# Kernel optimization log

Measured on AMD Instinct MI355X. Metric: run time of the kernel, lower is better.

The kernel has to match this reference:

```python
import jax, jax.numpy as jnp
import numpy as np

DIM = 2048
D_INNER = 2048
B = 4
T = 4096
INIT_DECAY = 0.5


def setup_inputs() -> dict:
    key = jax.random.key(0)
    k1, k2, k3 = jax.random.split(key, 3)
    x = jax.random.normal(k1, (B, T, DIM), dtype=jnp.float32)
    h0 = jnp.zeros((B, D_INNER), dtype=jnp.float32)
    # xavier_uniform for Linear(dim -> d_inner) and Linear(d_inner -> dim)
    lim_in = float(np.sqrt(6.0 / (DIM + D_INNER)))
    W_in = jax.random.uniform(k2, (D_INNER, DIM), minval=-lim_in, maxval=lim_in, dtype=jnp.float32)
    lim_out = float(np.sqrt(6.0 / (D_INNER + DIM)))
    W_out = jax.random.uniform(k3, (DIM, D_INNER), minval=-lim_out, maxval=lim_out, dtype=jnp.float32)
    init_log = float(np.log(INIT_DECAY / (1.0 - INIT_DECAY)))  # logit(0.5) = 0
    log_d = jnp.full((D_INNER,), init_log, dtype=jnp.float32)
    b = jnp.zeros((D_INNER,), dtype=jnp.float32)
    return {"x": x, "h0": h0, "W_in": W_in, "W_out": W_out, "log_d": log_d, "b": b}


def reference(x, h0, W_in, W_out, log_d, b):
    # x: [B, T, dim]
    d = jax.nn.sigmoid(log_d)                       # [D] per-dim decay in (0,1)
    xp = jax.nn.silu(jnp.einsum('btd,ed->bte', x, W_in))  # [B, T, D_inner]
    xs = jnp.swapaxes(xp, 0, 1)                     # [T, B, D]

    def step(h_prev, xt):
        h_new = d * (xt + h_prev) + b               # diagonal-decay recurrence
        out = h_new * jax.nn.silu(h_new)            # self-gating
        return h_new, out

    h_final, outs = jax.lax.scan(step, h0, xs)      # outs: [T, B, D]
    cell_out = jnp.swapaxes(outs, 0, 1)             # [B, T, D]
    output = jnp.einsum('bte,de->btd', cell_out, W_out)  # [B, T, dim]
    return output, h_final
```

## Files before the change

kernel.cpp:

```cpp
#include <hip/hip_runtime.h>
#include <hip/hip_bf16.h>

#define DIMV 2048
#define DIV  2048
#define BV   4
#define TV   4096
#define MV   (BV * TV)
#define GK   2048
#define NCH  64
#define CH   64

typedef __bf16 bf16x8 __attribute__((ext_vector_type(8)));
typedef __bf16 bf16x4 __attribute__((ext_vector_type(4)));
typedef float  floatx4 __attribute__((ext_vector_type(4)));

__device__ __forceinline__ void gload_lds16(const void* g, void* l) {
    __builtin_amdgcn_global_load_lds((const __attribute__((address_space(1))) void*)g,
                                     (__attribute__((address_space(3))) void*)l,
                                     16, 0, 0);
}

__global__ __launch_bounds__(256) void cvt_all(const float4* __restrict__ x,
                                               const float4* __restrict__ wi,
                                               const float4* __restrict__ wo,
                                               ushort4* __restrict__ xb,
                                               ushort4* __restrict__ wib,
                                               ushort4* __restrict__ wob) {
    int i = blockIdx.x * 256 + threadIdx.x;
    const float4* src;
    ushort4* dst;
    int off;
    if (i < 8388608)       { src = x;  dst = xb;  off = 0; }
    else if (i < 9437184)  { src = wi; dst = wib; off = 8388608; }
    else                   { src = wo; dst = wob; off = 9437184; }
    float4 v = src[i - off];
    __hip_bfloat16 a = __float2bfloat16(v.x);
    __hip_bfloat16 b = __float2bfloat16(v.y);
    __hip_bfloat16 c = __float2bfloat16(v.z);
    __hip_bfloat16 d = __float2bfloat16(v.w);
    ushort4 o;
    o.x = *(unsigned short*)&a;
    o.y = *(unsigned short*)&b;
    o.z = *(unsigned short*)&c;
    o.w = *(unsigned short*)&d;
    dst[i - off] = o;
}

template <int EPI>
__global__ __launch_bounds__(256) void gemm128_bt(const __hip_bfloat16* __restrict__ A,
                                                  const __hip_bfloat16* __restrict__ Bt,
                                                  float* __restrict__ Cf,
                                                  __hip_bfloat16* __restrict__ Cb) {
    __shared__ __align__(16) short As[2 * 128 * 32];
    __shared__ __align__(16) short Bs[2 * 128 * 32];

    const int tid  = threadIdx.x;
    const int lane = tid & 63;
    const int wave = tid >> 6;
    const int wm   = (wave >> 1) * 64;
    const int wn   = (wave & 1) * 64;
    const int lr   = lane & 15;
    const int lq   = lane >> 4;

    const int num_n = gridDim.x;
    const int p     = blockIdx.y * num_n + blockIdx.x;
    const int GM    = 8;
    const int grp   = p / (GM * num_n);
    const int rem   = p % (GM * num_n);
    const int m0    = (grp * GM + (rem % GM)) * 128;
    const int n0    = (rem / GM) * 128;

    const __hip_bfloat16* Aps[4];
    const __hip_bfloat16* Bps[4];
    short* Ald[4];
    short* Bld[4];
#pragma unroll
    for (int q = 0; q < 4; ++q) {
        const int j    = wave * 4 + q;
        const int pan  = j & 1;
        const int r0   = (j >> 1) * 16;
        const int row  = r0 + (lane >> 2);
        const int col  = pan * 32 + (lane & 3) * 8;
        Aps[q] = A  + (size_t)(m0 + row) * GK + col;
        Bps[q] = Bt + (size_t)(n0 + row) * GK + col;
        Ald[q] = &As[pan * 4096 + r0 * 32 + lane * 8];
        Bld[q] = &Bs[pan * 4096 + r0 * 32 + lane * 8];
    }

    floatx4 acc[4][4];
#pragma unroll
    for (int i = 0; i < 4; ++i)
#pragma unroll
        for (int j = 0; j < 4; ++j) acc[i][j] = 0.f;

    for (int k0 = 0; k0 < GK; k0 += 64) {
#pragma unroll
        for (int q = 0; q < 4; ++q) {
            gload_lds16(Aps[q] + k0, Ald[q]);
            gload_lds16(Bps[q] + k0, Bld[q]);
        }
        __syncthreads();

#pragma unroll
        for (int s = 0; s < 2; ++s) {
            bf16x8 af[4], bfr[4];
#pragma unroll
            for (int i = 0; i < 4; ++i)
                af[i] = *(const bf16x8*)&As[s * 4096 + (wm + i * 16 + lr) * 32 + lq * 8];
#pragma unroll
            for (int j = 0; j < 4; ++j)
                bfr[j] = *(const bf16x8*)&Bs[s * 4096 + (wn + j * 16 + lr) * 32 + lq * 8];
#pragma unroll
            for (int i = 0; i < 4; ++i)
#pragma unroll
                for (int j = 0; j < 4; ++j)
                    acc[i][j] = __builtin_amdgcn_mfma_f32_16x16x32_bf16(af[i], bfr[j], acc[i][j], 0, 0, 0);
        }
        __syncthreads();
    }

#pragma unroll
    for (int i = 0; i < 4; ++i) {
#pragma unroll
        for (int r = 0; r < 4; ++r) {
            const int row = m0 + wm + i * 16 + lq * 4 + r;
#pragma unroll
            for (int j = 0; j < 4; ++j) {
                const int col = n0 + wn + j * 16 + lr;
                float v = acc[i][j][r];
                if (EPI == 1) {
                    float s = v / (1.f + __expf(-v));
                    Cb[(size_t)row * DIV + col] = __float2bfloat16(s);
                } else {
                    Cf[(size_t)row * DIMV + col] = v;
                }
            }
        }
    }
}

__global__ __launch_bounds__(256) void scan_carry(const __hip_bfloat16* __restrict__ xp,
                                                  const float* __restrict__ logd,
                                                  const float* __restrict__ bias,
                                                  float* __restrict__ carry) {
    const int eg = blockIdx.x * 256 + threadIdx.x;
    const int e0 = eg * 4;
    const int c = blockIdx.y;
    const int b = blockIdx.z;
    const float4 ld = ((const float4*)logd)[eg];
    const float4 bb = ((const float4*)bias)[eg];
    float dv[4] = {1.f / (1.f + __expf(-ld.x)), 1.f / (1.f + __expf(-ld.y)),
                   1.f / (1.f + __expf(-ld.z)), 1.f / (1.f + __expf(-ld.w))};
    float bv[4] = {bb.x, bb.y, bb.z, bb.w};
    const __hip_bfloat16* p = xp + ((size_t)(b * TV + c * CH)) * DIV + e0;
    float h[4] = {0.f, 0.f, 0.f, 0.f};
#pragma unroll 8
    for (int i = 0; i < CH; ++i) {
        bf16x4 v = *(const bf16x4*)(p + (size_t)i * DIV);
#pragma unroll
        for (int j = 0; j < 4; ++j)
            h[j] = dv[j] * ((float)v[j] + h[j]) + bv[j];
    }
    float4 o = {h[0], h[1], h[2], h[3]};
    *(float4*)&carry[((size_t)b * NCH + c) * DIV + e0] = o;
}

__global__ __launch_bounds__(256) void scan_apply(const __hip_bfloat16* __restrict__ xp,
                                                  const float* __restrict__ logd,
                                                  const float* __restrict__ bias,
                                                  const float* __restrict__ h0,
                                                  const float* __restrict__ carry,
                                                  __hip_bfloat16* __restrict__ cell,
                                                  float* __restrict__ hfin) {
    const int eg = blockIdx.x * 256 + threadIdx.x;
    const int e0 = eg * 4;
    const int c = blockIdx.y;
    const int b = blockIdx.z;
    const float4 ld = ((const float4*)logd)[eg];
    const float4 bb = ((const float4*)bias)[eg];
    float dv[4] = {1.f / (1.f + __expf(-ld.x)), 1.f / (1.f + __expf(-ld.y)),
                   1.f / (1.f + __expf(-ld.z)), 1.f / (1.f + __expf(-ld.w))};
    float bv[4] = {bb.x, bb.y, bb.z, bb.w};
    float dCH[4];
#pragma unroll
    for (int j = 0; j < 4; ++j) dCH[j] = __powf(dv[j], (float)CH);

    float4 H4 = *(const float4*)&h0[(size_t)b * DIV + e0];
    float H[4] = {H4.x, H4.y, H4.z, H4.w};
    for (int j = 0; j < c; ++j) {
        float4 cr = *(const float4*)&carry[((size_t)b * NCH + j) * DIV + e0];
#pragma unroll
        for (int q = 0; q < 4; ++q) H[q] = dCH[q] * H[q] + ((const float*)&cr)[q];
    }

    const size_t base = ((size_t)(b * TV + c * CH)) * DIV + e0;
    float h[4] = {H[0], H[1], H[2], H[3]};
#pragma unroll 4
    for (int i = 0; i < CH; ++i) {
        bf16x4 v = *(const bf16x4*)(xp + base + (size_t)i * DIV);
        ushort4 o;
        unsigned short* op = (unsigned short*)&o;
#pragma unroll
        for (int j = 0; j < 4; ++j) {
            h[j] = dv[j] * ((float)v[j] + h[j]) + bv[j];
            float cv = h[j] * (h[j] / (1.f + __expf(-h[j])));
            __hip_bfloat16 cb = __float2bfloat16(cv);
            op[j] = *(unsigned short*)&cb;
        }
        *(ushort4*)(cell + base + (size_t)i * DIV) = o;
    }
    if (c == NCH - 1) {
        float4 o = {h[0], h[1], h[2], h[3]};
        *(float4*)&hfin[(size_t)b * DIV + e0] = o;
    }
}

extern "C" void kernel_launch(void* const* d_in, const int* in_sizes, int n_in,
                              void* d_out, int out_size, void* d_ws, size_t ws_size,
                              hipStream_t stream) {
    const float* x     = (const float*)d_in[0];
    const float* h0    = (const float*)d_in[1];
    const float* W_in  = (const float*)d_in[2];
    const float* W_out = (const float*)d_in[3];
    const float* log_d = (const float*)d_in[4];
    const float* bias  = (const float*)d_in[5];

    float* out  = (float*)d_out;
    float* hfin = out + (size_t)BV * TV * DIMV;

    char* ws = (char*)d_ws;
    __hip_bfloat16* xb    = (__hip_bfloat16*)ws;
    __hip_bfloat16* cellb = xb;
    __hip_bfloat16* wib   = (__hip_bfloat16*)(ws + 67108864);
    __hip_bfloat16* wob   = (__hip_bfloat16*)(ws + 67108864 + 8388608);
    __hip_bfloat16* xpb   = (__hip_bfloat16*)(ws + 67108864 + 16777216);
    float*          carry = (float*)(ws + 134217728 + 16777216);

    {
        int n4 = 10485760;
        cvt_all<<<n4 / 256, 256, 0, stream>>>((const float4*)x, (const float4*)W_in,
                                              (const float4*)W_out,
                                              (ushort4*)xb, (ushort4*)wib, (ushort4*)wob);
    }

    gemm128_bt<1><<<dim3(DIV / 128, MV / 128), 256, 0, stream>>>(xb, wib, nullptr, xpb);

    scan_carry<<<dim3(DIV / 1024, NCH, BV), 256, 0, stream>>>(xpb, log_d, bias, carry);
    scan_apply<<<dim3(DIV / 1024, NCH, BV), 256, 0, stream>>>(xpb, log_d, bias, h0, carry, cellb, hfin);

    gemm128_bt<0><<<dim3(DIMV / 128, MV / 128), 256, 0, stream>>>(cellb, wob, out, nullptr);
}
```

Baseline: 613.2 us.

## Replace 128x128 GEMM with double-buffered 256x256 tile GEMM using 8 waves

Measured after the change: 591.5 us. 3.5% less time.

```diff
diff --git a/kernel.cpp b/kernel.cpp
--- a/kernel.cpp
+++ b/kernel.cpp
@@ -47,87 +47,122 @@
 }
 
 template <int EPI>
-__global__ __launch_bounds__(256) void gemm128_bt(const __hip_bfloat16* __restrict__ A,
-                                                  const __hip_bfloat16* __restrict__ Bt,
-                                                  float* __restrict__ Cf,
-                                                  __hip_bfloat16* __restrict__ Cb) {
-    __shared__ __align__(16) short As[2 * 128 * 32];
-    __shared__ __align__(16) short Bs[2 * 128 * 32];
+__global__ __launch_bounds__(512, 2) void gemm256_bt(const __hip_bfloat16* __restrict__ A,
+                                                     const __hip_bfloat16* __restrict__ Bt,
+                                                     float* __restrict__ Cf,
+                                                     __hip_bfloat16* __restrict__ Cb) {
+    __shared__ __align__(16) short As[32768];
+    __shared__ __align__(16) short Bs[32768];
 
     const int tid  = threadIdx.x;
     const int lane = tid & 63;
     const int wave = tid >> 6;
-    const int wm   = (wave >> 1) * 64;
-    const int wn   = (wave & 1) * 64;
+    const int wm   = (wave >> 2) * 128;
+    const int wn   = (wave & 3) * 64;
     const int lr   = lane & 15;
     const int lq   = lane >> 4;
 
-    const int num_n = gridDim.x;
-    const int p     = blockIdx.y * num_n + blockIdx.x;
-    const int GM    = 8;
-    const int grp   = p / (GM * num_n);
-    const int rem   = p % (GM * num_n);
-    const int m0    = (grp * GM + (rem % GM)) * 128;
-    const int n0    = (rem / GM) * 128;
-
-    const __hip_bfloat16* Aps[4];
-    const __hip_bfloat16* Bps[4];
-    short* Ald[4];
-    short* Bld[4];
-#pragma unroll
-    for (int q = 0; q < 4; ++q) {
-        const int j    = wave * 4 + q;
-        const int pan  = j & 1;
-        const int r0   = (j >> 1) * 16;
-        const int row  = r0 + (lane >> 2);
-        const int col  = pan * 32 + (lane & 3) * 8;
-        Aps[q] = A  + (size_t)(m0 + row) * GK + col;
-        Bps[q] = Bt + (size_t)(n0 + row) * GK + col;
-        Ald[q] = &As[pan * 4096 + r0 * 32 + lane * 8];
-        Bld[q] = &Bs[pan * 4096 + r0 * 32 + lane * 8];
-    }
-
-    floatx4 acc[4][4];
-#pragma unroll
-    for (int i = 0; i < 4; ++i)
+    const int p   = blockIdx.y * gridDim.x + blockIdx.x;
+    const int swz = (p & 7) * 64 + (p >> 3);
+    const int m0  = (swz >> 3) * 256;
+    const int n0  = (swz & 7) * 256;
+
+    const int trow = tid >> 2;
+    const int tcol = (tid & 3) * 8;
+    const __hip_bfloat16* aG = A  + (size_t)(m0 + trow) * GK + tcol;
+    const __hip_bfloat16* bG = Bt + (size_t)(n0 + trow) * GK + tcol;
+    short* aL = As + tid * 8;
+    short* bL = Bs + tid * 8;
+
+#define STAGE(T_, C_) do {                                                    \
+    const size_t ko_ = (size_t)(T_) * 64;                                     \
+    short* al_ = aL + (C_) * 16384;                                           \
+    short* bl_ = bL + (C_) * 16384;                                           \
+    gload_lds16(aG + ko_,                         al_);                       \
+    gload_lds16(aG + ko_ + 32,                    al_ + 8192);                \
+    gload_lds16(aG + ko_ + (size_t)128 * GK,      al_ + 4096);                \
+    gload_lds16(aG + ko_ + (size_t)128 * GK + 32, al_ + 12288);               \
+    gload_lds16(bG + ko_,                         bl_);                       \
+    gload_lds16(bG + ko_ + 32,                    bl_ + 8192);                \
+    gload_lds16(bG + ko_ + (size_t)128 * GK,      bl_ + 4096);                \
+    gload_lds16(bG + ko_ + (size_t)128 * GK + 32, bl_ + 12288);               \
+} while (0)
+
+    floatx4 acc[8][4];
+#pragma unroll
+    for (int i = 0; i < 8; ++i)
 #pragma unroll
         for (int j = 0; j < 4; ++j) acc[i][j] = 0.f;
 
-    for (int k0 = 0; k0 < GK; k0 += 64) {
-#pragma unroll
-        for (int q = 0; q < 4; ++q) {
-            gload_lds16(Aps[q] + k0, Ald[q]);
-            gload_lds16(Bps[q] + k0, Bld[q]);
-        }
-        __syncthreads();
-
-#pragma unroll
-        for (int s = 0; s < 2; ++s) {
-            bf16x8 af[4], bfr[4];
-#pragma unroll
-            for (int i = 0; i < 4; ++i)
-                af[i] = *(const bf16x8*)&As[s * 4096 + (wm + i * 16 + lr) * 32 + lq * 8];
-#pragma unroll
-            for (int j = 0; j < 4; ++j)
-                bfr[j] = *(const bf16x8*)&Bs[s * 4096 + (wn + j * 16 + lr) * 32 + lq * 8];
-#pragma unroll
-            for (int i = 0; i < 4; ++i)
-#pragma unroll
-                for (int j = 0; j < 4; ++j)
-                    acc[i][j] = __builtin_amdgcn_mfma_f32_16x16x32_bf16(af[i], bfr[j], acc[i][j], 0, 0, 0);
-        }
-        __syncthreads();
-    }
-
-#pragma unroll
-    for (int i = 0; i < 4; ++i) {
+    STAGE(0, 0);
+    STAGE(1, 1);
+    asm volatile("s_waitcnt vmcnt(8)" ::: "memory");
+    asm volatile("s_barrier" ::: "memory");
+
+    const int aRd = (wm + lr) * 32 + lq * 8;
+    const int bRd = (wn + lr) * 32 + lq * 8;
+
+#define KSTEP(T_, DO_STAGE_, VM8_, VM0_) do {                                 \
+    const int c_ = (T_) & 1;                                                  \
+    const short* aP = As + c_ * 16384;                                        \
+    const short* bP = Bs + c_ * 16384;                                        \
+    bf16x8 afr[8][2], bfr[4][2];                                              \
+    _Pragma("unroll") for (int s = 0; s < 2; ++s) {                           \
+        _Pragma("unroll") for (int ni = 0; ni < 4; ++ni)                      \
+            bfr[ni][s] = *(const bf16x8*)&bP[bRd + s * 8192 + ni * 512];      \
+        _Pragma("unroll") for (int mi = 0; mi < 8; ++mi)                      \
+            afr[mi][s] = *(const bf16x8*)&aP[aRd + s * 8192 + mi * 512];      \
+    }                                                                         \
+    __builtin_amdgcn_s_setprio(1);                                            \
+    _Pragma("unroll") for (int mi = 0; mi < 4; ++mi)                          \
+        _Pragma("unroll") for (int ni = 0; ni < 4; ++ni)                      \
+            _Pragma("unroll") for (int s = 0; s < 2; ++s)                     \
+                acc[mi][ni] = __builtin_amdgcn_mfma_f32_16x16x32_bf16(        \
+                    afr[mi][s], bfr[ni][s], acc[mi][ni], 0, 0, 0);            \
+    _Pragma("unroll") for (int mi = 4; mi < 8; ++mi)                          \
+        _Pragma("unroll") for (int ni = 0; ni < 2; ++ni)                      \
+            _Pragma("unroll") for (int s = 0; s < 2; ++s)                     \
+                acc[mi][ni] = __builtin_amdgcn_mfma_f32_16x16x32_bf16(        \
+                    afr[mi][s], bfr[ni][s], acc[mi][ni], 0, 0, 0);            \
+    __builtin_amdgcn_s_setprio(0);                                            \
+           \
+    asm volatile("s_waitcnt lgkmcnt(0)" ::: "memory");                        \
+    asm volatile("s_barrier" ::: "memory");                                   \
+    if (DO_STAGE_) STAGE((T_) + 2, c_);                                       \
+    __builtin_amdgcn_s_setprio(1);                                            \
+    _Pragma("unroll") for (int mi = 4; mi < 8; ++mi)                          \
+        _Pragma("unroll") for (int ni = 2; ni < 4; ++ni)                      \
+            _Pragma("unroll") for (int s = 0; s < 2; ++s)                     \
+                acc[mi][ni] = __builtin_amdgcn_mfma_f32_16x16x32_bf16(        \
+                    afr[mi][s], bfr[ni][s], acc[mi][ni], 0, 0, 0);            \
+    __builtin_amdgcn_s_setprio(0);                                            \
+    if (VM8_) {                                                               \
+        asm volatile("s_waitcnt vmcnt(8)" ::: "memory");                      \
+        asm volatile("s_barrier" ::: "memory");                               \
+    }                                                                         \
+    if (VM0_) {                                                               \
+        asm volatile("s_waitcnt vmcnt(0)" ::: "memory");                      \
+        asm volatile("s_barrier" ::: "memory");                               \
+    }                                                                         \
+} while (0)
+
+#pragma unroll 2
+    for (int t = 0; t < 30; ++t) KSTEP(t, 1, 1, 0);
+    KSTEP(30, 0, 0, 1);
+    KSTEP(31, 0, 0, 0);
+
+#undef KSTEP
+#undef STAGE
+
+#pragma unroll
+    for (int mi = 0; mi < 8; ++mi) {
 #pragma unroll
         for (int r = 0; r < 4; ++r) {
-            const int row = m0 + wm + i * 16 + lq * 4 + r;
-#pragma unroll
-            for (int j = 0; j < 4; ++j) {
-                const int col = n0 + wn + j * 16 + lr;
-                float v = acc[i][j][r];
+            const int row = m0 + wm + mi * 16 + lq * 4 + r;
+#pragma unroll
+            for (int ni = 0; ni < 4; ++ni) {
+                const int col = n0 + wn + ni * 16 + lr;
+                float v = acc[mi][ni][r];
                 if (EPI == 1) {
                     float s = v / (1.f + __expf(-v));
                     Cb[(size_t)row * DIV + col] = __float2bfloat16(s);
@@ -243,10 +278,10 @@
                                               (ushort4*)xb, (ushort4*)wib, (ushort4*)wob);
     }
 
-    gemm128_bt<1><<<dim3(DIV / 128, MV / 128), 256, 0, stream>>>(xb, wib, nullptr, xpb);
+    gemm256_bt<1><<<dim3(DIV / 256, MV / 256), 512, 0, stream>>>(xb, wib, nullptr, xpb);
 
     scan_carry<<<dim3(DIV / 1024, NCH, BV), 256, 0, stream>>>(xpb, log_d, bias, carry);
     scan_apply<<<dim3(DIV / 1024, NCH, BV), 256, 0, stream>>>(xpb, log_d, bias, h0, carry, cellb, hfin);
 
-    gemm128_bt<0><<<dim3(DIMV / 128, MV / 128), 256, 0, stream>>>(cellb, wob, out, nullptr);
-}
+    gemm256_bt<0><<<dim3(DIMV / 256, MV / 256), 512, 0, stream>>>(cellb, wob, out, nullptr);
+}
```

## Replace 128x128 GEMM with pipelined 256x256 tile, swizzled LDS, 8 waves

Applied to the files above, without the earlier changes.

Result: faster. 590.8 us (-3.6%).

```diff
diff --git a/kernel.cpp b/kernel.cpp
--- a/kernel.cpp
+++ b/kernel.cpp
@@ -47,87 +47,155 @@
 }
 
 template <int EPI>
-__global__ __launch_bounds__(256) void gemm128_bt(const __hip_bfloat16* __restrict__ A,
-                                                  const __hip_bfloat16* __restrict__ Bt,
-                                                  float* __restrict__ Cf,
-                                                  __hip_bfloat16* __restrict__ Cb) {
-    __shared__ __align__(16) short As[2 * 128 * 32];
-    __shared__ __align__(16) short Bs[2 * 128 * 32];
+__global__ __launch_bounds__(512, 2) void gemm256_bt(const __hip_bfloat16* __restrict__ A,
+                                                     const __hip_bfloat16* __restrict__ Bt,
+                                                     float* __restrict__ Cf,
+                                                     __hip_bfloat16* __restrict__ Cb) {
+    __shared__ __align__(16) char AsB[65536];
+    __shared__ __align__(16) char BsB[65536];
 
     const int tid  = threadIdx.x;
     const int lane = tid & 63;
     const int wave = tid >> 6;
-    const int wm   = (wave >> 1) * 64;
-    const int wn   = (wave & 1) * 64;
+    const int wmh  = wave >> 2;
+    const int wnh  = (wave >> 1) & 1;
+    const int wno  = wave & 1;
     const int lr   = lane & 15;
     const int lq   = lane >> 4;
 
-    const int num_n = gridDim.x;
-    const int p     = blockIdx.y * num_n + blockIdx.x;
-    const int GM    = 8;
-    const int grp   = p / (GM * num_n);
-    const int rem   = p % (GM * num_n);
-    const int m0    = (grp * GM + (rem % GM)) * 128;
-    const int n0    = (rem / GM) * 128;
-
-    const __hip_bfloat16* Aps[4];
-    const __hip_bfloat16* Bps[4];
-    short* Ald[4];
-    short* Bld[4];
-#pragma unroll
-    for (int q = 0; q < 4; ++q) {
-        const int j    = wave * 4 + q;
-        const int pan  = j & 1;
-        const int r0   = (j >> 1) * 16;
-        const int row  = r0 + (lane >> 2);
-        const int col  = pan * 32 + (lane & 3) * 8;
-        Aps[q] = A  + (size_t)(m0 + row) * GK + col;
-        Bps[q] = Bt + (size_t)(n0 + row) * GK + col;
-        Ald[q] = &As[pan * 4096 + r0 * 32 + lane * 8];
-        Bld[q] = &Bs[pan * 4096 + r0 * 32 + lane * 8];
-    }
-
-    floatx4 acc[4][4];
-#pragma unroll
-    for (int i = 0; i < 4; ++i)
+    const int p   = blockIdx.y * gridDim.x + blockIdx.x;
+    const int swz = (p & 7) * 64 + (p >> 3);
+    const int m0  = (swz >> 3) * 256;
+    const int n0  = (swz & 7) * 256;
+
+    const int flip  = ((lr >> 2) & 1) << 5;
+    const int rdswz = lr * 128 + ((lq * 16) ^ flip);
+    const char* aRd0 = AsB + wmh * 16384 + rdswz;
+    const char* bRd0 = BsB + wnh * 16384 + wno * 8192 + rdswz;
+
+    const int ptid = tid ^ (((tid >> 5) & 1) << 1);
+    const int srow = ptid >> 3;
+    const int scol = (ptid & 7) * 8;
+    const __hip_bfloat16* aS_h0g0 = A  + (size_t)(m0 +   0 +  0 + srow) * GK + scol;
+    const __hip_bfloat16* aS_h0g1 = A  + (size_t)(m0 +   0 + 64 + srow) * GK + scol;
+    const __hip_bfloat16* aS_h1g0 = A  + (size_t)(m0 + 128 +  0 + srow) * GK + scol;
+    const __hip_bfloat16* aS_h1g1 = A  + (size_t)(m0 + 128 + 64 + srow) * GK + scol;
+    const __hip_bfloat16* bS_h0g0 = Bt + (size_t)(n0 +   0 +  0 + srow) * GK + scol;
+    const __hip_bfloat16* bS_h0g1 = Bt + (size_t)(n0 +   0 + 64 + srow) * GK + scol;
+    const __hip_bfloat16* bS_h1g0 = Bt + (size_t)(n0 + 128 +  0 + srow) * GK + scol;
+    const __hip_bfloat16* bS_h1g1 = Bt + (size_t)(n0 + 128 + 64 + srow) * GK + scol;
+
+#define BARR  asm volatile("s_barrier" ::: "memory")
+#define WAITL do { asm volatile("s_waitcnt lgkmcnt(0)" ::: "memory");          \
+                   __builtin_amdgcn_sched_barrier(0); } while (0)
+#define VMW(N_) asm volatile("s_waitcnt vmcnt(" #N_ ")" ::: "memory")
+
+#define STG(SRC_, DST_, T_) gload_lds16((SRC_) + (size_t)(T_) * 64, (DST_))
+#define ST_AG0(T_, C_) do {                                                    \
+    STG(aS_h0g0, AsB + (C_) * 32768 +     0 + tid * 16, T_);                   \
+    STG(aS_h1g0, AsB + (C_) * 32768 + 16384 + tid * 16, T_); } while (0)
+#define ST_AG1(T_, C_) do {                                                    \
+    STG(aS_h0g1, AsB + (C_) * 32768 +  8192 + tid * 16, T_);                   \
+    STG(aS_h1g1, AsB + (C_) * 32768 + 24576 + tid * 16, T_); } while (0)
+#define ST_BG0(T_, C_) do {                                                    \
+    STG(bS_h0g0, BsB + (C_) * 32768 +     0 + tid * 16, T_);                   \
+    STG(bS_h1g0, BsB + (C_) * 32768 + 16384 + tid * 16, T_); } while (0)
+#define ST_BG1(T_, C_) do {                                                    \
+    STG(bS_h0g1, BsB + (C_) * 32768 +  8192 + tid * 16, T_);                   \
+    STG(bS_h1g1, BsB + (C_) * 32768 + 24576 + tid * 16, T_); } while (0)
+
+#define RDPH_A(DST_, MI0_, C_)                                                 \
+    _Pragma("unroll") for (int mi_ = 0; mi_ < 4; ++mi_)                        \
+      _Pragma("unroll") for (int s_ = 0; s_ < 2; ++s_)                         \
+        DST_[mi_][s_] = *(const bf16x8*)(aRd0 + (C_) * 32768 +                 \
+                                         ((MI0_) + mi_) * 2048 + s_ * 64);
+#define RDPH_B(DST_, NI0_, C_)                                                 \
+    _Pragma("unroll") for (int ni_ = 0; ni_ < 2; ++ni_)                        \
+      _Pragma("unroll") for (int s_ = 0; s_ < 2; ++s_)                         \
+        DST_[ni_][s_] = *(const bf16x8*)(bRd0 + (C_) * 32768 +                 \
+                                         ((NI0_) + ni_) * 2048 + s_ * 64);
+
+#define QUAD(MI0_, NI0_, AF_, BF_)                                             \
+    __builtin_amdgcn_s_setprio(1);                                             \
+    _Pragma("unroll") for (int mi_ = 0; mi_ < 4; ++mi_)                        \
+      _Pragma("unroll") for (int ni_ = 0; ni_ < 2; ++ni_)                      \
+        _Pragma("unroll") for (int s_ = 0; s_ < 2; ++s_)                       \
+          acc[(MI0_) + mi_][(NI0_) + ni_] =                                    \
+            __builtin_amdgcn_mfma_f32_16x16x32_bf16(                           \
+              AF_[mi_][s_], BF_[ni_][s_],                                      \
+              acc[(MI0_) + mi_][(NI0_) + ni_], 0, 0, 0);                       \
+    __builtin_amdgcn_s_setprio(0);
+
+#define KTILE(T_, C_, MODE_) do {                                              \
+    bf16x8 a03[4][2], a47[4][2], b01[2][2], b23[2][2];                         \
+                                                        \
+    RDPH_A(a03, 0, C_);                                                        \
+    RDPH_B(b01, 0, C_);                                                        \
+    if ((MODE_) >= 1) { ST_BG1((T_) + 1, (C_) ^ 1); }                          \
+    BARR; WAITL;                                                               \
+    QUAD(0, 0, a03, b01);                                                      \
+    VMW(8); BARR;                                                              \
+                                                        \
+    RDPH_B(b23, 2, C_);                                                        \
+    if ((MODE_) == 1) { ST_AG0((T_) + 2, C_); }                                \
+    BARR; WAITL;                                                               \
+    QUAD(0, 2, a03, b23);                                                      \
+    VMW(4); BARR;                                                              \
+                                                        \
+    RDPH_A(a47, 4, C_);                                                        \
+    if ((MODE_) == 1) { ST_BG0((T_) + 2, C_); }                                \
+    BARR; WAITL;                                                               \
+    QUAD(4, 2, a47, b23);                                                      \
+    BARR;                                                                      \
+                                                        \
+    if ((MODE_) == 1) { ST_AG1((T_) + 2, C_); }                                \
+    BARR;                                                                      \
+    QUAD(4, 0, a47, b01);                                                      \
+    if ((MODE_) == 2) { VMW(0); } else { VMW(6); }                             \
+    BARR;                                                                      \
+} while (0)
+
+    floatx4 acc[8][4];
+#pragma unroll
+    for (int i = 0; i < 8; ++i)
 #pragma unroll
         for (int j = 0; j < 4; ++j) acc[i][j] = 0.f;
 
-    for (int k0 = 0; k0 < GK; k0 += 64) {
-#pragma unroll
-        for (int q = 0; q < 4; ++q) {
-            gload_lds16(Aps[q] + k0, Ald[q]);
-            gload_lds16(Bps[q] + k0, Bld[q]);
-        }
-        __syncthreads();
-
-#pragma unroll
-        for (int s = 0; s < 2; ++s) {
-            bf16x8 af[4], bfr[4];
-#pragma unroll
-            for (int i = 0; i < 4; ++i)
-                af[i] = *(const bf16x8*)&As[s * 4096 + (wm + i * 16 + lr) * 32 + lq * 8];
-#pragma unroll
-            for (int j = 0; j < 4; ++j)
-                bfr[j] = *(const bf16x8*)&Bs[s * 4096 + (wn + j * 16 + lr) * 32 + lq * 8];
-#pragma unroll
-            for (int i = 0; i < 4; ++i)
-#pragma unroll
-                for (int j = 0; j < 4; ++j)
-                    acc[i][j] = __builtin_amdgcn_mfma_f32_16x16x32_bf16(af[i], bfr[j], acc[i][j], 0, 0, 0);
-        }
-        __syncthreads();
-    }
-
-#pragma unroll
-    for (int i = 0; i < 4; ++i) {
+    ST_AG0(0, 0); ST_BG0(0, 0); ST_AG1(0, 0); ST_BG1(0, 0);
+    ST_AG0(1, 1); ST_BG0(1, 1); ST_AG1(1, 1);
+    VMW(6); BARR;
+
+    for (int t2 = 0; t2 < 15; ++t2) {
+        KTILE(2 * t2,     0, 1);
+        KTILE(2 * t2 + 1, 1, 1);
+    }
+    KTILE(30, 0, 2);
+    KTILE(31, 1, 0);
+
+#undef KTILE
+#undef QUAD
+#undef RDPH_A
+#undef RDPH_B
+#undef ST_AG0
+#undef ST_AG1
+#undef ST_BG0
+#undef ST_BG1
+#undef STG
+#undef VMW
+#undef WAITL
+#undef BARR
+
+    const int wm = wmh * 128;
+    const int wn = (wave & 3) * 64;
+#pragma unroll
+    for (int mi = 0; mi < 8; ++mi) {
 #pragma unroll
         for (int r = 0; r < 4; ++r) {
-            const int row = m0 + wm + i * 16 + lq * 4 + r;
-#pragma unroll
-            for (int j = 0; j < 4; ++j) {
-                const int col = n0 + wn + j * 16 + lr;
-                float v = acc[i][j][r];
+            const int row = m0 + wm + mi * 16 + lq * 4 + r;
+#pragma unroll
+            for (int ni = 0; ni < 4; ++ni) {
+                const int col = n0 + wn + ni * 16 + lr;
+                float v = acc[mi][ni][r];
                 if (EPI == 1) {
                     float s = v / (1.f + __expf(-v));
                     Cb[(size_t)row * DIV + col] = __float2bfloat16(s);
@@ -243,10 +311,10 @@
                                               (ushort4*)xb, (ushort4*)wib, (ushort4*)wob);
     }
 
-    gemm128_bt<1><<<dim3(DIV / 128, MV / 128), 256, 0, stream>>>(xb, wib, nullptr, xpb);
+    gemm256_bt<1><<<dim3(DIV / 256, MV / 256), 512, 0, stream>>>(xb, wib, nullptr, xpb);
 
     scan_carry<<<dim3(DIV / 1024, NCH, BV), 256, 0, stream>>>(xpb, log_d, bias, carry);
     scan_apply<<<dim3(DIV / 1024, NCH, BV), 256, 0, stream>>>(xpb, log_d, bias, h0, carry, cellb, hfin);
 
-    gemm128_bt<0><<<dim3(DIMV / 128, MV / 128), 256, 0, stream>>>(cellb, wob, out, nullptr);
-}
+    gemm256_bt<0><<<dim3(DIMV / 256, MV / 256), 512, 0, stream>>>(cellb, wob, out, nullptr);
+}
```
